# Optimization experiments

Hardware: AMD Instinct MI355X
Metric: run time of the kernel (lower is better)

The kernel has to match this reference:

```python
import jax, jax.numpy as jnp
import numpy as np

B, T, V = 128, 64, 10000
NI, ENC_NH, DEC_NH, NZ = 512, 640, 1024, 128
ND, K, D = 8, 1024, 160  # num_dicts, codebook size, per-dict embed dim (2*ENC_NH/ND)
BETA = 0.25


def _lstm(xg, Whh, h0, c0):
    """Run an LSTM given precomputed input-gate activations xg: (B,T,4H).
    Torch gate order: i, f, g, o. Returns (outputs (B,T,H), hT, cT)."""
    def step(carry, xt):
        h, c = carry
        g = xt + h @ Whh.T
        i, f, gg, o = jnp.split(g, 4, axis=-1)
        c = jax.nn.sigmoid(f) * c + jax.nn.sigmoid(i) * jnp.tanh(gg)
        h = jax.nn.sigmoid(o) * jnp.tanh(c)
        return (h, c), h
    (hT, cT), hs = jax.lax.scan(step, (h0, c0), jnp.swapaxes(xg, 0, 1))
    return jnp.swapaxes(hs, 0, 1), hT, cT


def setup_inputs() -> dict:
    key = jax.random.key(0)
    ks = jax.random.split(key, 20)
    s = 0.05
    inp = {
        "x": jax.random.randint(ks[0], (B, T), 0, V),
        "enc_embed": jax.random.normal(ks[1], (V, NI)) * s,
        "enc_Wih_f": jax.random.normal(ks[2], (4 * ENC_NH, NI)) * s,
        "enc_Whh_f": jax.random.normal(ks[3], (4 * ENC_NH, ENC_NH)) * s,
        "enc_b_f": jnp.zeros((4 * ENC_NH,)),
        "enc_Wih_b": jax.random.normal(ks[4], (4 * ENC_NH, NI)) * s,
        "enc_Whh_b": jax.random.normal(ks[5], (4 * ENC_NH, ENC_NH)) * s,
        "enc_b_b": jnp.zeros((4 * ENC_NH,)),
        "enc_lin": jax.random.normal(ks[6], (2 * NZ, 2 * ENC_NH)) * s,
        "z2dec_W": jax.random.normal(ks[7], (DEC_NH, NZ)) * s,
        "z2dec_b": jnp.zeros((DEC_NH,)),
        "codebooks": jax.random.uniform(ks[8], (ND, K, D), minval=-1.0 / K, maxval=1.0 / K),
        "suffix_W": jax.random.normal(ks[9], (NI, 2 * ENC_NH)) * s,
        "dec_embed": jax.random.normal(ks[10], (V, NI)) * s,
        "dec_Wih": jax.random.normal(ks[11], (4 * DEC_NH, NI)) * s,
        "dec_Whh": jax.random.normal(ks[12], (4 * DEC_NH, DEC_NH)) * s,
        "dec_b": jnp.zeros((4 * DEC_NH,)),
        "pred_W": jax.random.normal(ks[13], (V, DEC_NH)) * s,
    }
    return inp


def reference(x, enc_embed, enc_Wih_f, enc_Whh_f, enc_b_f, enc_Wih_b, enc_Whh_b,
              enc_b_b, enc_lin, z2dec_W, z2dec_b, codebooks, suffix_W,
              dec_embed, dec_Wih, dec_Whh, dec_b, pred_W):
    sg = jax.lax.stop_gradient
    Bsz = x.shape[0]
    z0e = jnp.zeros((Bsz, ENC_NH), enc_embed.dtype)

    # ---- bidirectional LSTM encoder ----
    we = enc_embed[x]  # (B,T,NI)
    xg_f = jnp.einsum('bti,gi->btg', we, enc_Wih_f) + enc_b_f
    xg_b = jnp.einsum('bti,gi->btg', we[:, ::-1], enc_Wih_b) + enc_b_b
    _, hf, _ = _lstm(xg_f, enc_Whh_f, z0e, z0e)
    _, hb, _ = _lstm(xg_b, enc_Whh_b, z0e, z0e)
    fhs = jnp.concatenate([hf, hb], axis=-1)  # (B, 2*ENC_NH)

    mu, logvar = jnp.split(fhs @ enc_lin.T, 2, axis=-1)  # (B,NZ) each
    kl = 0.5 * jnp.sum(mu ** 2 + jnp.exp(logvar) - logvar - 1.0, axis=1)

    root = mu @ z2dec_W.T + z2dec_b  # (B, DEC_NH) -- eval path: z = mu

    # ---- vector quantization over ND codebook slices of fhs ----
    lat = fhs.reshape(Bsz, ND, D)
    dist = (jnp.sum(lat ** 2, -1, keepdims=True)
            + jnp.sum(codebooks ** 2, -1)[None]
            - 2.0 * jnp.einsum('bnd,nkd->bnk', lat, codebooks))  # (B,ND,K)
    inds = jnp.argmin(dist, axis=-1)  # (B,ND)
    q = codebooks[jnp.arange(ND)[None, :], inds]  # (B,ND,D) gather lookup
    commit = jnp.mean((sg(q) - lat) ** 2, axis=-1)
    embl = jnp.mean((q - sg(lat)) ** 2, axis=-1)
    vq_loss = jnp.sum(embl + BETA * commit, axis=-1)  # (B,)
    q_st = (lat + sg(q - lat)).reshape(Bsz, ND * D)  # straight-through

    # ---- LSTM decoder ----
    suffix = q_st @ suffix_W.T  # (B, NI)
    demb = dec_embed[x] + suffix[:, None, :]
    xg_d = jnp.einsum('bti,gi->btg', demb, dec_Wih) + dec_b
    dec_out, _, _ = _lstm(xg_d, dec_Whh, jnp.tanh(root), root)
    logits = jnp.einsum('btd,vd->btv', dec_out, pred_W)  # (B,T,V)
    return logits, vq_loss, kl, inds
```

## Files before the change

### kernel.cpp

```cpp
#include <hip/hip_runtime.h>


typedef unsigned short u16;
typedef unsigned int u32;

__device__ __forceinline__ float b2f(u16 u) {
    union { u32 i; float f; } v; v.i = ((u32)u) << 16; return v.f;
}
__device__ __forceinline__ u16 f2b(float f) {
    union { float f; u32 i; } v; v.f = f;
    u32 x = v.i;
    u32 r = x + 0x7FFFu + ((x >> 16) & 1u);
    return (u16)(r >> 16);
}
__device__ __forceinline__ float sigmoidf(float x) {
    return 1.0f / (1.0f + expf(-x));
}
__device__ __forceinline__ float ldin(const void* p, size_t i, int bf) {
    return bf ? b2f(((const u16*)p)[i]) : ((const float*)p)[i];
}
__device__ __forceinline__ void stout(void* p, size_t i, float v, int bf) {
    if (bf) ((u16*)p)[i] = f2b(v); else ((float*)p)[i] = v;
}

__global__ void probe_dtype(const void* emb, int* flag)
{
    __shared__ int cnt[128];
    int tid = threadIdx.x;
    u16 u = ((const u16*)emb)[2 * tid];
    int e = (u >> 7) & 0xFF;
    cnt[tid] = (e >= 100 && e <= 127) ? 1 : 0;
    __syncthreads();
    for (int s = 64; s > 0; s >>= 1) {
        if (tid < s) cnt[tid] += cnt[tid + s];
        __syncthreads();
    }
    if (tid == 0) *flag = (cnt[0] >= 96) ? 1 : 0;
}

__global__ void zero_kernel(float* p, int n)
{
    int i = blockIdx.x * 256 + threadIdx.x;
    if (i < n) p[i] = 0.0f;
}

template <int FINAL>
__global__ __launch_bounds__(256) void gemm_kernel(
    const float* __restrict__ A, int lda,
    const void* __restrict__ Wv,
    const void* __restrict__ biasv,
    void* __restrict__ Cv, int ldc,
    int M, int N, int K, const int* __restrict__ flagp)
{
    __shared__ float As[16][68];
    __shared__ float Ws[16][68];

    const int bf   = *flagp;
    const int tid  = threadIdx.x;
    const int tx   = tid & 15;
    const int ty   = tid >> 4;
    const int row0 = blockIdx.y << 6;
    const int col0 = blockIdx.x << 6;
    const int lm   = tid >> 2;
    const int lk   = (tid & 3) << 2;

    const float* Ap = A + (size_t)(row0 + lm) * lda + lk;
    const int wn    = col0 + lm;
    const bool wok  = wn < N;
    const size_t woff = (size_t)(wok ? wn : 0) * K + lk;

    float acc[4][4];
#pragma unroll
    for (int i = 0; i < 4; i++)
#pragma unroll
        for (int j = 0; j < 4; j++) acc[i][j] = 0.0f;

    for (int kt = 0; kt < K; kt += 16) {
        float4 av = *reinterpret_cast<const float4*>(Ap + kt);
        float w0 = 0.f, w1 = 0.f, w2 = 0.f, w3 = 0.f;
        if (wok) {
            if (bf) {
                ushort4 wv = *reinterpret_cast<const ushort4*>((const u16*)Wv + woff + kt);
                w0 = b2f(wv.x); w1 = b2f(wv.y); w2 = b2f(wv.z); w3 = b2f(wv.w);
            } else {
                float4 wv = *reinterpret_cast<const float4*>((const float*)Wv + woff + kt);
                w0 = wv.x; w1 = wv.y; w2 = wv.z; w3 = wv.w;
            }
        }
        As[lk + 0][lm] = av.x; As[lk + 1][lm] = av.y;
        As[lk + 2][lm] = av.z; As[lk + 3][lm] = av.w;
        Ws[lk + 0][lm] = w0; Ws[lk + 1][lm] = w1;
        Ws[lk + 2][lm] = w2; Ws[lk + 3][lm] = w3;
        __syncthreads();
#pragma unroll
        for (int kk = 0; kk < 16; kk++) {
            float a4[4], b4[4];
#pragma unroll
            for (int i = 0; i < 4; i++) a4[i] = As[kk][(ty << 2) + i];
#pragma unroll
            for (int j = 0; j < 4; j++) b4[j] = Ws[kk][(tx << 2) + j];
#pragma unroll
            for (int i = 0; i < 4; i++)
#pragma unroll
                for (int j = 0; j < 4; j++) acc[i][j] += a4[i] * b4[j];
        }
        __syncthreads();
    }

#pragma unroll
    for (int i = 0; i < 4; i++) {
        const int r = row0 + (ty << 2) + i;
#pragma unroll
        for (int j = 0; j < 4; j++) {
            const int cc = col0 + (tx << 2) + j;
            if (cc < N) {
                float v = acc[i][j];
                if (biasv) v += ldin(biasv, cc, bf);
                if (FINAL) stout(Cv, (size_t)r * ldc + cc, v, bf);
                else       ((float*)Cv)[(size_t)r * ldc + cc] = v;
            }
        }
    }
}

__global__ void gather_enc(const int* __restrict__ x, const void* __restrict__ emb,
                           float* __restrict__ we, float* __restrict__ werev,
                           const int* __restrict__ flagp)
{
    int bf = *flagp;
    int idx = blockIdx.x * 256 + threadIdx.x;
    int r = idx >> 9, i = idx & 511;
    float v = ldin(emb, (size_t)x[r] * 512 + i, bf);
    we[idx] = v;
    int b = r >> 6, t = r & 63;
    werev[(((size_t)(b * 64 + (63 - t))) << 9) + i] = v;
}

__global__ void demb_kernel(const int* __restrict__ x, const void* __restrict__ emb,
                            const float* __restrict__ suffix, float* __restrict__ out,
                            const int* __restrict__ flagp)
{
    int bf = *flagp;
    int idx = blockIdx.x * 256 + threadIdx.x;
    int r = idx >> 9, i = idx & 511;
    out[idx] = ldin(emb, (size_t)x[r] * 512 + i, bf) + suffix[((size_t)(r >> 6) << 9) + i];
}

__global__ void lstm_gate(const float* __restrict__ gbuf, const float* __restrict__ xg,
                          float* __restrict__ h, float* __restrict__ c,
                          float* __restrict__ outh, int H, int t, int T)
{
    int idx = blockIdx.x * 256 + threadIdx.x;
    if (idx >= 128 * H) return;
    int b = idx / H, j = idx - b * H;
    const float* xr = xg + (size_t)(b * T + t) * (4 * H);
    const float* gr = gbuf + (size_t)b * (4 * H);
    float gi = gr[j]         + xr[j];
    float gf = gr[H + j]     + xr[H + j];
    float gg = gr[2 * H + j] + xr[2 * H + j];
    float go = gr[3 * H + j] + xr[3 * H + j];
    float cv = sigmoidf(gf) * c[idx] + sigmoidf(gi) * tanhf(gg);
    float hv = sigmoidf(go) * tanhf(cv);
    c[idx] = cv;
    h[idx] = hv;
    if (outh) outh[(size_t)(b * T + t) * H + j] = hv;
}

__global__ void copy_h(const float* __restrict__ h, float* __restrict__ fhs, int H, int off)
{
    int idx = blockIdx.x * 256 + threadIdx.x;
    if (idx >= 128 * H) return;
    int b = idx / H, j = idx - b * H;
    fhs[b * 1280 + off + j] = h[idx];
}

__global__ void dec_init(const float* __restrict__ root, float* __restrict__ h, float* __restrict__ c)
{
    int idx = blockIdx.x * 256 + threadIdx.x;
    float r = root[idx];
    h[idx] = tanhf(r);
    c[idx] = r;
}

__global__ void kl_kernel(const float* __restrict__ ml, void* __restrict__ outv,
                          const int* __restrict__ flagp)
{
    const size_t OFF_KL = 81920128;
    int b = blockIdx.x, j = threadIdx.x;
    float mu = ml[b * 256 + j];
    float lv = ml[b * 256 + 128 + j];
    float v = mu * mu + expf(lv) - lv - 1.0f;
    __shared__ float red[128];
    red[j] = v; __syncthreads();
    for (int s = 64; s > 0; s >>= 1) {
        if (j < s) red[j] += red[j + s];
        __syncthreads();
    }
    if (j == 0) stout(outv, OFF_KL + b, 0.5f * red[0], *flagp);
}

__global__ __launch_bounds__(256) void vq_kernel(
    const float* __restrict__ fhs, const void* __restrict__ cbs,
    float* __restrict__ q, float* __restrict__ vq_accum, void* __restrict__ outv,
    const int* __restrict__ flagp)
{
    const size_t OFF_IND = 81920256;
    int bf = *flagp;
    int bn = blockIdx.x;
    int b = bn >> 3, n = bn & 7;
    __shared__ float lat[160];
    __shared__ float ssc[256];
    __shared__ int   sid[256];
    __shared__ float slat2;
    __shared__ int   bestk;
    int tid = threadIdx.x;
    if (tid < 160) lat[tid] = fhs[b * 1280 + n * 160 + tid];
    __syncthreads();
    ssc[tid] = (tid < 160) ? lat[tid] * lat[tid] : 0.0f;
    __syncthreads();
    for (int s = 128; s > 0; s >>= 1) {
        if (tid < s) ssc[tid] += ssc[tid + s];
        __syncthreads();
    }
    if (tid == 0) slat2 = ssc[0];
    __syncthreads();
    float l2 = slat2;

    float best = 3.4e38f; int bi = 0;
    for (int k = tid; k < 1024; k += 256) {
        size_t cbase = (size_t)(n * 1024 + k) * 160;
        float dot = 0.0f, c2 = 0.0f;
        for (int d = 0; d < 160; d++) {
            float f = ldin(cbs, cbase + d, bf);
            dot += lat[d] * f;
            c2  += f * f;
        }
        float s = l2 + c2 - 2.0f * dot;
        if (s < best) { best = s; bi = k; }
    }
    ssc[tid] = best; sid[tid] = bi;
    __syncthreads();
    for (int s = 128; s > 0; s >>= 1) {
        if (tid < s) {
            float o = ssc[tid + s]; int oi = sid[tid + s];
            if (o < ssc[tid] || (o == ssc[tid] && oi < sid[tid])) { ssc[tid] = o; sid[tid] = oi; }
        }
        __syncthreads();
    }
    if (tid == 0) { bestk = sid[0]; stout(outv, OFF_IND + bn, (float)sid[0], bf); }
    __syncthreads();

    float part = 0.0f;
    if (tid < 160) {
        float qv = ldin(cbs, (size_t)(n * 1024 + bestk) * 160 + tid, bf);
        q[b * 1280 + n * 160 + tid] = qv;
        float df = qv - lat[tid];
        part = df * df;
    }
    ssc[tid] = part;
    __syncthreads();
    for (int s = 128; s > 0; s >>= 1) {
        if (tid < s) ssc[tid] += ssc[tid + s];
        __syncthreads();
    }
    if (tid == 0) atomicAdd(&vq_accum[b], ssc[0]);
}

__global__ void vq_fin(const float* __restrict__ vq_accum, void* __restrict__ outv,
                       const int* __restrict__ flagp)
{
    const size_t OFF_VQ = 81920000;
    int b = threadIdx.x;
    stout(outv, OFF_VQ + b, vq_accum[b] * (1.25f / 160.0f), *flagp);
}


extern "C" void kernel_launch(void* const* d_in, const int* in_sizes, int n_in,
                              void* d_out, int out_size, void* d_ws, size_t ws_size,
                              hipStream_t stream)
{
    const int*  x         = (const int*)d_in[0];
    const void* enc_embed = d_in[1];
    const void* enc_Wih_f = d_in[2];
    const void* enc_Whh_f = d_in[3];
    const void* enc_b_f   = d_in[4];
    const void* enc_Wih_b = d_in[5];
    const void* enc_Whh_b = d_in[6];
    const void* enc_b_b   = d_in[7];
    const void* enc_lin   = d_in[8];
    const void* z2dec_W   = d_in[9];
    const void* z2dec_b   = d_in[10];
    const void* codebooks = d_in[11];
    const void* suffix_W  = d_in[12];
    const void* dec_embed = d_in[13];
    const void* dec_Wih   = d_in[14];
    const void* dec_Whh   = d_in[15];
    const void* dec_b     = d_in[16];
    const void* pred_W    = d_in[17];

    char* ob = (char*)d_out;
    float* xg    = (float*)(ob + 0);
    float* we    = (float*)(ob + 83886080);
    float* werev = (float*)(ob + 100663296);
    float* demb  = (float*)(ob + 134217728);

    char* wb = (char*)d_ws;
    float* decout = (float*)(wb + 0);
    float* g      = (float*)(wb + 33554432);
    float* h      = (float*)(wb + 35651584);
    float* c      = (float*)(wb + 36175872);
    float* fhs    = (float*)(wb + 36700160);
    float* ml     = (float*)(wb + 37355520);
    float* root   = (float*)(wb + 37486592);
    float* q      = (float*)(wb + 38010880);
    float* suffix = (float*)(wb + 38666240);
    float* vqa    = (float*)(wb + 38928384);
    int*   flag   = (int*)  (wb + 38928896);

    probe_dtype<<<1, 128, 0, stream>>>(enc_embed, flag);
    zero_kernel<<<1024, 256, 0, stream>>>(h, 262144);
    zero_kernel<<<1, 128, 0, stream>>>(vqa, 128);

    gather_enc<<<16384, 256, 0, stream>>>(x, enc_embed, we, werev, flag);

    gemm_kernel<0><<<dim3(40, 128), 256, 0, stream>>>(we, 512, enc_Wih_f, enc_b_f,
                                                      xg, 2560, 8192, 2560, 512, flag);
    for (int t = 0; t < 64; t++) {
        gemm_kernel<0><<<dim3(40, 2), 256, 0, stream>>>(h, 640, enc_Whh_f, nullptr,
                                                        g, 2560, 128, 2560, 640, flag);
        lstm_gate<<<320, 256, 0, stream>>>(g, xg, h, c, nullptr, 640, t, 64);
    }
    copy_h<<<320, 256, 0, stream>>>(h, fhs, 640, 0);

    zero_kernel<<<1024, 256, 0, stream>>>(h, 262144);
    gemm_kernel<0><<<dim3(40, 128), 256, 0, stream>>>(werev, 512, enc_Wih_b, enc_b_b,
                                                      xg, 2560, 8192, 2560, 512, flag);
    for (int t = 0; t < 64; t++) {
        gemm_kernel<0><<<dim3(40, 2), 256, 0, stream>>>(h, 640, enc_Whh_b, nullptr,
                                                        g, 2560, 128, 2560, 640, flag);
        lstm_gate<<<320, 256, 0, stream>>>(g, xg, h, c, nullptr, 640, t, 64);
    }
    copy_h<<<320, 256, 0, stream>>>(h, fhs, 640, 640);

    gemm_kernel<0><<<dim3(4, 2), 256, 0, stream>>>(fhs, 1280, enc_lin, nullptr,
                                                   ml, 256, 128, 256, 1280, flag);
    kl_kernel<<<128, 128, 0, stream>>>(ml, d_out, flag);

    gemm_kernel<0><<<dim3(16, 2), 256, 0, stream>>>(ml, 256, z2dec_W, z2dec_b,
                                                    root, 1024, 128, 1024, 128, flag);

    vq_kernel<<<1024, 256, 0, stream>>>(fhs, codebooks, q, vqa, d_out, flag);
    vq_fin<<<1, 128, 0, stream>>>(vqa, d_out, flag);

    gemm_kernel<0><<<dim3(8, 2), 256, 0, stream>>>(q, 1280, suffix_W, nullptr,
                                                   suffix, 512, 128, 512, 1280, flag);

    demb_kernel<<<16384, 256, 0, stream>>>(x, dec_embed, suffix, demb, flag);

    gemm_kernel<0><<<dim3(64, 128), 256, 0, stream>>>(demb, 512, dec_Wih, dec_b,
                                                      xg, 4096, 8192, 4096, 512, flag);

    dec_init<<<512, 256, 0, stream>>>(root, h, c);
    for (int t = 0; t < 64; t++) {
        gemm_kernel<0><<<dim3(64, 2), 256, 0, stream>>>(h, 1024, dec_Whh, nullptr,
                                                        g, 4096, 128, 4096, 1024, flag);
        lstm_gate<<<512, 256, 0, stream>>>(g, xg, h, c, decout, 1024, t, 64);
    }

    gemm_kernel<1><<<dim3(157, 128), 256, 0, stream>>>(decout, 1024, pred_W, nullptr,
                                                       d_out, 10000, 8192, 10000, 1024, flag);
}
```

Baseline: 13.78 ms.

## Fuse LSTM recurrent GEMM with gate update and add 128x128 register-tiled GEMM

Each LSTM timestep now runs a single kernel. It computes the four gate slices of h@Whh for a 16-unit column block and applies the cell update in the epilogue, using ping-pong h buffers so no separate gate kernel or g buffer round-trip is needed. The decoder writes h straight into decout and reads the previous step back from it. The large input-projection and output-logit GEMMs move to a new 128x128 tile kernel with 8x8 per-thread accumulators and vectorized stores, which raises arithmetic intensity. The cost is higher register pressure and fewer blocks for some shapes (pred GEMM N=10000 gives a partial last tile).

Result: faster. 12.32 ms (-10.6%).

```diff
diff --git a/kernel.cpp b/kernel.cpp
--- a/kernel.cpp
+++ b/kernel.cpp
@@ -123,6 +123,195 @@
     }
 }
 
+template <int FINAL>
+__global__ __launch_bounds__(256) void gemm128(
+    const float* __restrict__ A, int lda,
+    const void* __restrict__ Wv,
+    const void* __restrict__ biasv,
+    void* __restrict__ Cv, int ldc,
+    int M, int N, int K, const int* __restrict__ flagp)
+{
+    __shared__ float As[8][132];
+    __shared__ float Ws[8][132];
+
+    const int bf   = *flagp;
+    const int tid  = threadIdx.x;
+    const int tx   = tid & 15;
+    const int ty   = tid >> 4;
+    const int row0 = blockIdx.y << 7;
+    const int col0 = blockIdx.x << 7;
+    const int lr   = tid >> 1;
+    const int lk   = (tid & 1) << 2;
+
+    const float* Ap = A + (size_t)(row0 + lr) * lda + lk;
+    const int wn    = col0 + lr;
+    const bool wok  = wn < N;
+    const size_t woff = (size_t)(wok ? wn : 0) * K + lk;
+
+    float acc[8][8];
+#pragma unroll
+    for (int i = 0; i < 8; i++)
+#pragma unroll
+        for (int j = 0; j < 8; j++) acc[i][j] = 0.0f;
+
+    for (int kt = 0; kt < K; kt += 8) {
+        float4 av = *reinterpret_cast<const float4*>(Ap + kt);
+        float w0 = 0.f, w1 = 0.f, w2 = 0.f, w3 = 0.f;
+        if (wok) {
+            if (bf) {
+                ushort4 wv = *reinterpret_cast<const ushort4*>((const u16*)Wv + woff + kt);
+                w0 = b2f(wv.x); w1 = b2f(wv.y); w2 = b2f(wv.z); w3 = b2f(wv.w);
+            } else {
+                float4 wv = *reinterpret_cast<const float4*>((const float*)Wv + woff + kt);
+                w0 = wv.x; w1 = wv.y; w2 = wv.z; w3 = wv.w;
+            }
+        }
+        As[lk + 0][lr] = av.x; As[lk + 1][lr] = av.y;
+        As[lk + 2][lr] = av.z; As[lk + 3][lr] = av.w;
+        Ws[lk + 0][lr] = w0; Ws[lk + 1][lr] = w1;
+        Ws[lk + 2][lr] = w2; Ws[lk + 3][lr] = w3;
+        __syncthreads();
+#pragma unroll
+        for (int kk = 0; kk < 8; kk++) {
+            float4 av0 = *reinterpret_cast<const float4*>(&As[kk][ty << 3]);
+            float4 av1 = *reinterpret_cast<const float4*>(&As[kk][(ty << 3) + 4]);
+            float4 bv0 = *reinterpret_cast<const float4*>(&Ws[kk][tx << 3]);
+            float4 bv1 = *reinterpret_cast<const float4*>(&Ws[kk][(tx << 3) + 4]);
+            float a8[8] = {av0.x, av0.y, av0.z, av0.w, av1.x, av1.y, av1.z, av1.w};
+            float b8[8] = {bv0.x, bv0.y, bv0.z, bv0.w, bv1.x, bv1.y, bv1.z, bv1.w};
+#pragma unroll
+            for (int i = 0; i < 8; i++)
+#pragma unroll
+                for (int j = 0; j < 8; j++) acc[i][j] += a8[i] * b8[j];
+        }
+        __syncthreads();
+    }
+
+#pragma unroll
+    for (int i = 0; i < 8; i++) {
+        const size_t r = row0 + (ty << 3) + i;
+#pragma unroll
+        for (int jq = 0; jq < 2; jq++) {
+            const int cc = col0 + (tx << 3) + (jq << 2);
+            if (cc < N) {
+                float v0 = acc[i][jq * 4 + 0], v1 = acc[i][jq * 4 + 1];
+                float v2 = acc[i][jq * 4 + 2], v3 = acc[i][jq * 4 + 3];
+                if (biasv) {
+                    v0 += ldin(biasv, cc + 0, bf); v1 += ldin(biasv, cc + 1, bf);
+                    v2 += ldin(biasv, cc + 2, bf); v3 += ldin(biasv, cc + 3, bf);
+                }
+                if (FINAL && bf) {
+                    ushort4 o; o.x = f2b(v0); o.y = f2b(v1); o.z = f2b(v2); o.w = f2b(v3);
+                    *reinterpret_cast<ushort4*>((u16*)Cv + r * ldc + cc) = o;
+                } else {
+                    float4 o; o.x = v0; o.y = v1; o.z = v2; o.w = v3;
+                    *reinterpret_cast<float4*>((float*)Cv + r * ldc + cc) = o;
+                }
+            }
+        }
+    }
+}
+
+__global__ __launch_bounds__(256) void lstm_step(
+    const float* __restrict__ hin, int hin_rs,
+    const void* __restrict__ Whh,
+    const float* __restrict__ xg,
+    float* __restrict__ c,
+    float* __restrict__ hout, int hout_rs,
+    int H, int t, int T, const int* __restrict__ flagp)
+{
+    __shared__ float smem[4352];
+    float (*As)[68] = (float (*)[68])smem;
+    float (*Ws)[68] = (float (*)[68])(smem + 2176);
+    float (*Cs)[68] = (float (*)[68])smem;
+
+    const int bf   = *flagp;
+    const int tid  = threadIdx.x;
+    const int tx   = tid & 15;
+    const int ty   = tid >> 4;
+    const int row0 = blockIdx.y << 6;
+    const int j0   = blockIdx.x << 4;
+    const int lm   = tid >> 2;
+    const int lk   = (tid & 3) << 2;
+
+    const float* Ap = hin + (size_t)(row0 + lm) * hin_rs;
+    const int gate  = lm >> 4;
+    const int jj    = lm & 15;
+    const size_t wbase = (size_t)(gate * H + j0 + jj) * H;
+
+    float acc[4][4];
+#pragma unroll
+    for (int i = 0; i < 4; i++)
+#pragma unroll
+        for (int j = 0; j < 4; j++) acc[i][j] = 0.0f;
+
+    for (int kt = 0; kt < H; kt += 32) {
+        float4 a0 = *reinterpret_cast<const float4*>(Ap + kt + lk);
+        float4 a1 = *reinterpret_cast<const float4*>(Ap + kt + lk + 16);
+        float w0[4], w1[4];
+        if (bf) {
+            const u16* wp = (const u16*)Whh + wbase + kt + lk;
+            ushort4 u0 = *reinterpret_cast<const ushort4*>(wp);
+            ushort4 u1 = *reinterpret_cast<const ushort4*>(wp + 16);
+            w0[0] = b2f(u0.x); w0[1] = b2f(u0.y); w0[2] = b2f(u0.z); w0[3] = b2f(u0.w);
+            w1[0] = b2f(u1.x); w1[1] = b2f(u1.y); w1[2] = b2f(u1.z); w1[3] = b2f(u1.w);
+        } else {
+            const float* wp = (const float*)Whh + wbase + kt + lk;
+            float4 f0 = *reinterpret_cast<const float4*>(wp);
+            float4 f1 = *reinterpret_cast<const float4*>(wp + 16);
+            w0[0] = f0.x; w0[1] = f0.y; w0[2] = f0.z; w0[3] = f0.w;
+            w1[0] = f1.x; w1[1] = f1.y; w1[2] = f1.z; w1[3] = f1.w;
+        }
+        As[lk + 0][lm]  = a0.x; As[lk + 1][lm]  = a0.y;
+        As[lk + 2][lm]  = a0.z; As[lk + 3][lm]  = a0.w;
+        As[lk + 16][lm] = a1.x; As[lk + 17][lm] = a1.y;
+        As[lk + 18][lm] = a1.z; As[lk + 19][lm] = a1.w;
+        Ws[lk + 0][lm]  = w0[0]; Ws[lk + 1][lm]  = w0[1];
+        Ws[lk + 2][lm]  = w0[2]; Ws[lk + 3][lm]  = w0[3];
+        Ws[lk + 16][lm] = w1[0]; Ws[lk + 17][lm] = w1[1];
+        Ws[lk + 18][lm] = w1[2]; Ws[lk + 19][lm] = w1[3];
+        __syncthreads();
+#pragma unroll
+        for (int kk = 0; kk < 32; kk++) {
+            float4 av = *reinterpret_cast<const float4*>(&As[kk][ty << 2]);
+            float4 bv = *reinterpret_cast<const float4*>(&Ws[kk][tx << 2]);
+            float a4[4] = {av.x, av.y, av.z, av.w};
+            float b4[4] = {bv.x, bv.y, bv.z, bv.w};
+#pragma unroll
+            for (int i = 0; i < 4; i++)
+#pragma unroll
+                for (int j = 0; j < 4; j++) acc[i][j] += a4[i] * b4[j];
+        }
+        __syncthreads();
+    }
+
+#pragma unroll
+    for (int i = 0; i < 4; i++)
+#pragma unroll
+        for (int j = 0; j < 4; j++)
+            Cs[(ty << 2) + i][(tx << 2) + j] = acc[i][j];
+    __syncthreads();
+
+#pragma unroll
+    for (int rep = 0; rep < 4; rep++) {
+        const int idx = rep * 256 + tid;
+        const int rl  = idx >> 4;
+        const int j2  = idx & 15;
+        const int r   = row0 + rl;
+        const int j   = j0 + j2;
+        const float* xr = xg + (size_t)(r * T + t) * (4 * (size_t)H);
+        float gi = Cs[rl][j2]      + xr[j];
+        float gf = Cs[rl][16 + j2] + xr[H + j];
+        float gg = Cs[rl][32 + j2] + xr[2 * H + j];
+        float go = Cs[rl][48 + j2] + xr[3 * H + j];
+        const size_t ci = (size_t)r * H + j;
+        float cv = sigmoidf(gf) * c[ci] + sigmoidf(gi) * tanhf(gg);
+        float hv = sigmoidf(go) * tanhf(cv);
+        c[ci] = cv;
+        hout[(size_t)r * hout_rs + j] = hv;
+    }
+}
+
 __global__ void gather_enc(const int* __restrict__ x, const void* __restrict__ emb,
                            float* __restrict__ we, float* __restrict__ werev,
                            const int* __restrict__ flagp)
@@ -144,26 +333,6 @@
     int idx = blockIdx.x * 256 + threadIdx.x;
     int r = idx >> 9, i = idx & 511;
     out[idx] = ldin(emb, (size_t)x[r] * 512 + i, bf) + suffix[((size_t)(r >> 6) << 9) + i];
-}
-
-__global__ void lstm_gate(const float* __restrict__ gbuf, const float* __restrict__ xg,
-                          float* __restrict__ h, float* __restrict__ c,
-                          float* __restrict__ outh, int H, int t, int T)
-{
-    int idx = blockIdx.x * 256 + threadIdx.x;
-    if (idx >= 128 * H) return;
-    int b = idx / H, j = idx - b * H;
-    const float* xr = xg + (size_t)(b * T + t) * (4 * H);
-    const float* gr = gbuf + (size_t)b * (4 * H);
-    float gi = gr[j]         + xr[j];
-    float gf = gr[H + j]     + xr[H + j];
-    float gg = gr[2 * H + j] + xr[2 * H + j];
-    float go = gr[3 * H + j] + xr[3 * H + j];
-    float cv = sigmoidf(gf) * c[idx] + sigmoidf(gi) * tanhf(gg);
-    float hv = sigmoidf(go) * tanhf(cv);
-    c[idx] = cv;
-    h[idx] = hv;
-    if (outh) outh[(size_t)(b * T + t) * H + j] = hv;
 }
 
 __global__ void copy_h(const float* __restrict__ h, float* __restrict__ fhs, int H, int off)
@@ -306,41 +475,47 @@
 
     char* wb = (char*)d_ws;
     float* decout = (float*)(wb + 0);
-    float* g      = (float*)(wb + 33554432);
-    float* h      = (float*)(wb + 35651584);
-    float* c      = (float*)(wb + 36175872);
-    float* fhs    = (float*)(wb + 36700160);
-    float* ml     = (float*)(wb + 37355520);
-    float* root   = (float*)(wb + 37486592);
-    float* q      = (float*)(wb + 38010880);
-    float* suffix = (float*)(wb + 38666240);
-    float* vqa    = (float*)(wb + 38928384);
-    int*   flag   = (int*)  (wb + 38928896);
+    float* h0     = (float*)(wb + 33554432);
+    float* h1     = (float*)(wb + 34078720);
+    float* c      = (float*)(wb + 34603008);
+    float* fhs    = (float*)(wb + 35127296);
+    float* ml     = (float*)(wb + 35782656);
+    float* root   = (float*)(wb + 35913728);
+    float* q      = (float*)(wb + 36438016);
+    float* suffix = (float*)(wb + 37093376);
+    float* vqa    = (float*)(wb + 37355520);
+    int*   flag   = (int*)  (wb + 37356032);
 
     probe_dtype<<<1, 128, 0, stream>>>(enc_embed, flag);
-    zero_kernel<<<1024, 256, 0, stream>>>(h, 262144);
+    zero_kernel<<<1536, 256, 0, stream>>>(h0, 393216);
     zero_kernel<<<1, 128, 0, stream>>>(vqa, 128);
 
     gather_enc<<<16384, 256, 0, stream>>>(x, enc_embed, we, werev, flag);
 
-    gemm_kernel<0><<<dim3(40, 128), 256, 0, stream>>>(we, 512, enc_Wih_f, enc_b_f,
-                                                      xg, 2560, 8192, 2560, 512, flag);
-    for (int t = 0; t < 64; t++) {
-        gemm_kernel<0><<<dim3(40, 2), 256, 0, stream>>>(h, 640, enc_Whh_f, nullptr,
-                                                        g, 2560, 128, 2560, 640, flag);
-        lstm_gate<<<320, 256, 0, stream>>>(g, xg, h, c, nullptr, 640, t, 64);
-    }
-    copy_h<<<320, 256, 0, stream>>>(h, fhs, 640, 0);
-
-    zero_kernel<<<1024, 256, 0, stream>>>(h, 262144);
-    gemm_kernel<0><<<dim3(40, 128), 256, 0, stream>>>(werev, 512, enc_Wih_b, enc_b_b,
-                                                      xg, 2560, 8192, 2560, 512, flag);
-    for (int t = 0; t < 64; t++) {
-        gemm_kernel<0><<<dim3(40, 2), 256, 0, stream>>>(h, 640, enc_Whh_b, nullptr,
-                                                        g, 2560, 128, 2560, 640, flag);
-        lstm_gate<<<320, 256, 0, stream>>>(g, xg, h, c, nullptr, 640, t, 64);
-    }
-    copy_h<<<320, 256, 0, stream>>>(h, fhs, 640, 640);
+    gemm128<0><<<dim3(20, 64), 256, 0, stream>>>(we, 512, enc_Wih_f, enc_b_f,
+                                                 xg, 2560, 8192, 2560, 512, flag);
+    {
+        float* hp = h0; float* hn = h1;
+        for (int t = 0; t < 64; t++) {
+            lstm_step<<<dim3(40, 2), 256, 0, stream>>>(hp, 640, enc_Whh_f, xg, c,
+                                                       hn, 640, 640, t, 64, flag);
+            float* tmp = hp; hp = hn; hn = tmp;
+        }
+        copy_h<<<320, 256, 0, stream>>>(hp, fhs, 640, 0);
+    }
+
+    zero_kernel<<<1536, 256, 0, stream>>>(h0, 393216);
+    gemm128<0><<<dim3(20, 64), 256, 0, stream>>>(werev, 512, enc_Wih_b, enc_b_b,
+                                                 xg, 2560, 8192, 2560, 512, flag);
+    {
+        float* hp = h0; float* hn = h1;
+        for (int t = 0; t < 64; t++) {
+            lstm_step<<<dim3(40, 2), 256, 0, stream>>>(hp, 640, enc_Whh_b, xg, c,
+                                                       hn, 640, 640, t, 64, flag);
+            float* tmp = hp; hp = hn; hn = tmp;
+        }
+        copy_h<<<320, 256, 0, stream>>>(hp, fhs, 640, 640);
+    }
 
     gemm_kernel<0><<<dim3(4, 2), 256, 0, stream>>>(fhs, 1280, enc_lin, nullptr,
                                                    ml, 256, 128, 256, 1280, flag);
@@ -357,16 +532,18 @@
 
     demb_kernel<<<16384, 256, 0, stream>>>(x, dec_embed, suffix, demb, flag);
 
-    gemm_kernel<0><<<dim3(64, 128), 256, 0, stream>>>(demb, 512, dec_Wih, dec_b,
-                                                      xg, 4096, 8192, 4096, 512, flag);
-
-    dec_init<<<512, 256, 0, stream>>>(root, h, c);
+    gemm128<0><<<dim3(32, 64), 256, 0, stream>>>(demb, 512, dec_Wih, dec_b,
+                                                 xg, 4096, 8192, 4096, 512, flag);
+
+    dec_init<<<512, 256, 0, stream>>>(root, h0, c);
     for (int t = 0; t < 64; t++) {
-        gemm_kernel<0><<<dim3(64, 2), 256, 0, stream>>>(h, 1024, dec_Whh, nullptr,
-                                                        g, 4096, 128, 4096, 1024, flag);
-        lstm_gate<<<512, 256, 0, stream>>>(g, xg, h, c, decout, 1024, t, 64);
-    }
-
-    gemm_kernel<1><<<dim3(157, 128), 256, 0, stream>>>(decout, 1024, pred_W, nullptr,
-                                                       d_out, 10000, 8192, 10000, 1024, flag);
-}
+        const float* hin = (t == 0) ? h0 : (decout + (size_t)(t - 1) * 1024);
+        const int hrs    = (t == 0) ? 1024 : 65536;
+        lstm_step<<<dim3(64, 2), 256, 0, stream>>>(hin, hrs, dec_Whh, xg, c,
+                                                   decout + (size_t)t * 1024, 65536,
+                                                   1024, t, 64, flag);
+    }
+
+    gemm128<1><<<dim3(79, 64), 256, 0, stream>>>(decout, 1024, pred_W, nullptr,
+                                                 d_out, 10000, 8192, 10000, 1024, flag);
+}
```
